# Kernel tuning notes

Measured on AMD Instinct MI355X. Metric: run time of the kernel, lower is better.

The kernel has to match this reference:

```python
import jax, jax.numpy as jnp
import numpy as np

INPUT_SIZE = 20
HIDDEN = 51
OUT = 1
B = 4096
T = 512


def _init_lstm_params(key, in_dim, hid_dim):
    # PyTorch LSTMCell init: U(-1/sqrt(hid), 1/sqrt(hid))
    k = 1.0 / np.sqrt(hid_dim)
    ks = jax.random.split(key, 4)
    W_ih = jax.random.uniform(ks[0], (4 * hid_dim, in_dim), minval=-k, maxval=k, dtype=jnp.float32)
    W_hh = jax.random.uniform(ks[1], (4 * hid_dim, hid_dim), minval=-k, maxval=k, dtype=jnp.float32)
    b_ih = jax.random.uniform(ks[2], (4 * hid_dim,), minval=-k, maxval=k, dtype=jnp.float32)
    b_hh = jax.random.uniform(ks[3], (4 * hid_dim,), minval=-k, maxval=k, dtype=jnp.float32)
    return W_ih, W_hh, b_ih, b_hh


def setup_inputs() -> dict:
    key = jax.random.key(0)
    k_x, k1, k2, k3, k4 = jax.random.split(key, 5)
    x = jax.random.normal(k_x, (B, T, INPUT_SIZE), dtype=jnp.float32)
    W_ih1, W_hh1, b_ih1, b_hh1 = _init_lstm_params(k1, INPUT_SIZE, HIDDEN)
    W_ih2, W_hh2, b_ih2, b_hh2 = _init_lstm_params(k2, HIDDEN, OUT)
    kl = 1.0 / np.sqrt(OUT)
    ka, kb, kc, kd = jax.random.split(k3, 4)
    W_mu = jax.random.uniform(ka, (OUT, OUT), minval=-kl, maxval=kl, dtype=jnp.float32)
    b_mu = jax.random.uniform(kb, (OUT,), minval=-kl, maxval=kl, dtype=jnp.float32)
    W_lv = jax.random.uniform(kc, (OUT, OUT), minval=-kl, maxval=kl, dtype=jnp.float32)
    b_lv = jax.random.uniform(kd, (OUT,), minval=-kl, maxval=kl, dtype=jnp.float32)
    return {
        "x": x,
        "W_ih1": W_ih1, "W_hh1": W_hh1, "b_ih1": b_ih1, "b_hh1": b_hh1,
        "W_ih2": W_ih2, "W_hh2": W_hh2, "b_ih2": b_ih2, "b_hh2": b_hh2,
        "W_mu": W_mu, "b_mu": b_mu, "W_lv": W_lv, "b_lv": b_lv,
    }


def _lstm_cell(x_t, h, c, W_ih, W_hh, b_ih, b_hh):
    # PyTorch LSTMCell: gate order i, f, g, o
    gates = x_t @ W_ih.T + b_ih + h @ W_hh.T + b_hh
    i, f, g, o = jnp.split(gates, 4, axis=-1)
    c_new = jax.nn.sigmoid(f) * c + jax.nn.sigmoid(i) * jnp.tanh(g)
    h_new = jax.nn.sigmoid(o) * jnp.tanh(c_new)
    return h_new, c_new


def reference(x, W_ih1, W_hh1, b_ih1, b_hh1, W_ih2, W_hh2, b_ih2, b_hh2, W_mu, b_mu, W_lv, b_lv):
    bsz = x.shape[0]
    h1 = jnp.zeros((bsz, HIDDEN), dtype=x.dtype)
    c1 = jnp.zeros((bsz, HIDDEN), dtype=x.dtype)
    h2 = jnp.zeros((bsz, OUT), dtype=x.dtype)
    c2 = jnp.zeros((bsz, OUT), dtype=x.dtype)

    def step(carry, x_t):
        h1, c1, h2, c2 = carry
        h1, c1 = _lstm_cell(x_t, h1, c1, W_ih1, W_hh1, b_ih1, b_hh1)
        h2, c2 = _lstm_cell(h1, h2, c2, W_ih2, W_hh2, b_ih2, b_hh2)
        return (h1, c1, h2, c2), h2

    xs = jnp.swapaxes(x, 0, 1)  # [T, B, input_size]
    _, h2_seq = jax.lax.scan(step, (h1, c1, h2, c2), xs)  # h2_seq: [T, B, 1]
    agg = jnp.mean(h2_seq, axis=0)  # [B, 1] mean over time
    mu = agg @ W_mu.T + b_mu
    log_var = agg @ W_lv.T + b_lv
    sigma = jnp.exp(0.5 * log_var)
    lower = mu - 1.96 * sigma
    upper = mu + 1.96 * sigma
    return (lower, mu, upper, log_var)
```

## Files before the change

### kernel.cpp

```cpp
#include <hip/hip_runtime.h>

#define B_TOT 4096
#define T_STEPS 512
#define IN 20
#define HID 51

typedef float f32x4 __attribute__((ext_vector_type(4)));
typedef short s16x8 __attribute__((ext_vector_type(8)));

__device__ __forceinline__ unsigned short f2bf(float f) {
    unsigned int u = __float_as_uint(f);
    unsigned int r = (u + 0x7fffu + ((u >> 16) & 1u)) >> 16;
    return (unsigned short)r;
}

__device__ __forceinline__ float fast_rcp(float x) { return __builtin_amdgcn_rcpf(x); }
__device__ __forceinline__ float sigf(float x) { return fast_rcp(1.0f + __expf(-x)); }
__device__ __forceinline__ float tanh_(float x) { return 1.0f - 2.0f * fast_rcp(1.0f + __expf(2.0f * x)); }


__global__ __launch_bounds__(512, 2)
void lstm_fused(const float* __restrict__ x,
                const float* __restrict__ Wih1, const float* __restrict__ Whh1,
                const float* __restrict__ bih1, const float* __restrict__ bhh1,
                const float* __restrict__ Wih2, const float* __restrict__ Whh2,
                const float* __restrict__ bih2, const float* __restrict__ bhh2,
                const float* __restrict__ Wmu,  const float* __restrict__ bmu,
                const float* __restrict__ Wlv,  const float* __restrict__ blv,
                float* __restrict__ out)
{
    __shared__ __align__(16) unsigned short vA[2][3][64][8];

    const int tid  = threadIdx.x;
    const int lane = tid & 63;
    const int w    = tid >> 6;
    const int bidx = blockIdx.x;

    const int ntile = (w < 6) ? 2 : 1;
    int tiles[2];
    tiles[0] = (w < 6) ? 2 * w : (w == 6 ? 12 : 13);
    tiles[1] = (w < 6) ? 2 * w + 1 : -1;
    const bool isL2 = (tiles[0] == 13);

    s16x8 wfrag[2][3];
    float bias[2][4];
    #pragma unroll
    for (int ti = 0; ti < 2; ++ti) {
        const int tau = tiles[ti];
        const int m = lane & 15;
        #pragma unroll
        for (int ks = 0; ks < 3; ++ks) {
            s16x8 f;
            #pragma unroll
            for (int j = 0; j < 8; ++j) {
                int k = ks * 32 + ((lane >> 4) << 3) + j;
                float v = 0.0f;
                if (tau >= 0) {
                    if (tau < 13) {
                        int g = m & 3, unit = tau * 4 + (m >> 2);
                        if (unit < HID) {
                            int row = g * HID + unit;
                            if (k < IN) v = Wih1[row * IN + k];
                            else if (k >= 32 && k < 32 + HID) v = Whh1[row * HID + (k - 32)];
                        }
                    } else {
                        if (m < 4 && k >= 32 && k < 32 + HID) v = Wih2[m * HID + (k - 32)];
                    }
                }
                f[j] = (short)f2bf(v);
            }
            wfrag[ti][ks] = f;
        }
        #pragma unroll
        for (int r = 0; r < 4; ++r) {
            float bv = 0.0f;
            if (tau >= 0 && tau < 13) {
                int unit = tau * 4 + (lane >> 4);
                if (unit < HID) bv = bih1[r * HID + unit] + bhh1[r * HID + unit];
            }
            bias[ti][r] = bv;
        }
    }

    float whh2g[4], b2g[4];
    #pragma unroll
    for (int r = 0; r < 4; ++r) { whh2g[r] = Whh2[r]; b2g[r] = bih2[r] + bhh2[r]; }

    const bool xs = (tid < 16 * IN);
    const int xb = tid / IN, xm = tid % IN;
    const float* xp = x + ((size_t)(bidx * 16 + xb) * T_STEPS) * IN + xm;
    const int xrow = ((xm >> 3) & 3) * 16 + xb;
    const int xj = xm & 7;

    {
        unsigned short* vz = &vA[0][0][0][0];
        for (int i = tid; i < 2 * 3 * 64 * 8; i += 512) vz[i] = 0;
    }
    __syncthreads();
    if (xs) vA[0][0][xrow][xj] = f2bf(xp[0]);
    __syncthreads();

    float c1[2] = {0.f, 0.f};
    float c2p = 0.f, h2p = 0.f, sum2 = 0.f;

    for (int t = 0; t < T_STEPS; ++t) {
        const int p  = t & 1;
        const int pn = p ^ 1;

        const int t1 = (t < T_STEPS - 1) ? t + 1 : t;
        float xr = 0.0f;
        if (xs) xr = xp[(size_t)t1 * IN];

        s16x8 bf0 = *(const s16x8*)&vA[p][0][lane][0];
        s16x8 bf1 = *(const s16x8*)&vA[p][1][lane][0];
        s16x8 bf2 = *(const s16x8*)&vA[p][2][lane][0];

        f32x4 acc[2];
        {
            f32x4 a = {0.f, 0.f, 0.f, 0.f};
            a = __builtin_amdgcn_mfma_f32_16x16x32_bf16(wfrag[0][0], bf0, a, 0, 0, 0);
            a = __builtin_amdgcn_mfma_f32_16x16x32_bf16(wfrag[0][1], bf1, a, 0, 0, 0);
            a = __builtin_amdgcn_mfma_f32_16x16x32_bf16(wfrag[0][2], bf2, a, 0, 0, 0);
            acc[0] = a;
        }
        if (ntile == 2) {
            f32x4 a = {0.f, 0.f, 0.f, 0.f};
            a = __builtin_amdgcn_mfma_f32_16x16x32_bf16(wfrag[1][0], bf0, a, 0, 0, 0);
            a = __builtin_amdgcn_mfma_f32_16x16x32_bf16(wfrag[1][1], bf1, a, 0, 0, 0);
            a = __builtin_amdgcn_mfma_f32_16x16x32_bf16(wfrag[1][2], bf2, a, 0, 0, 0);
            acc[1] = a;
        }

        #pragma unroll
        for (int ti = 0; ti < 2; ++ti) {
            if (ti < ntile && tiles[ti] < 13) {
                float gi = acc[ti][0] + bias[ti][0];
                float gf = acc[ti][1] + bias[ti][1];
                float gg = acc[ti][2] + bias[ti][2];
                float go = acc[ti][3] + bias[ti][3];
                float c  = sigf(gf) * c1[ti] + sigf(gi) * tanh_(gg);
                c1[ti]   = c;
                float h  = sigf(go) * tanh_(c);
                int unit = tiles[ti] * 4 + (lane >> 4);
                int k    = 32 + unit;
                int b    = lane & 15;
                vA[pn][k >> 5][(((k >> 3) & 3) << 4) + b][k & 7] = f2bf(h);
            }
        }

        if (isL2 && t > 0 && lane < 16) {
            float pi = acc[0][0] + b2g[0] + whh2g[0] * h2p;
            float pf = acc[0][1] + b2g[1] + whh2g[1] * h2p;
            float pg = acc[0][2] + b2g[2] + whh2g[2] * h2p;
            float po = acc[0][3] + b2g[3] + whh2g[3] * h2p;
            float c2 = sigf(pf) * c2p + sigf(pi) * tanh_(pg);
            c2p = c2;
            h2p = sigf(po) * tanh_(c2);
            sum2 += h2p;
        }

        if (xs) vA[pn][0][xrow][xj] = f2bf(xr);

        __syncthreads();
    }

    if (isL2) {
        s16x8 bf0 = *(const s16x8*)&vA[0][0][lane][0];
        s16x8 bf1 = *(const s16x8*)&vA[0][1][lane][0];
        s16x8 bf2 = *(const s16x8*)&vA[0][2][lane][0];
        f32x4 a = {0.f, 0.f, 0.f, 0.f};
        a = __builtin_amdgcn_mfma_f32_16x16x32_bf16(wfrag[0][0], bf0, a, 0, 0, 0);
        a = __builtin_amdgcn_mfma_f32_16x16x32_bf16(wfrag[0][1], bf1, a, 0, 0, 0);
        a = __builtin_amdgcn_mfma_f32_16x16x32_bf16(wfrag[0][2], bf2, a, 0, 0, 0);
        if (lane < 16) {
            float pi = a[0] + b2g[0] + whh2g[0] * h2p;
            float pf = a[1] + b2g[1] + whh2g[1] * h2p;
            float pg = a[2] + b2g[2] + whh2g[2] * h2p;
            float po = a[3] + b2g[3] + whh2g[3] * h2p;
            float c2 = sigf(pf) * c2p + sigf(pi) * tanh_(pg);
            h2p = sigf(po) * tanh_(c2);
            sum2 += h2p;

            float agg = sum2 * (1.0f / 512.0f);
            float mu  = Wmu[0] * agg + bmu[0];
            float lv  = Wlv[0] * agg + blv[0];
            float sg  = __expf(0.5f * lv);
            int bg = bidx * 16 + lane;
            out[bg]             = mu - 1.96f * sg;
            out[B_TOT + bg]     = mu;
            out[2 * B_TOT + bg] = mu + 1.96f * sg;
            out[3 * B_TOT + bg] = lv;
        }
    }
}

extern "C" void kernel_launch(void* const* d_in, const int* in_sizes, int n_in,
                              void* d_out, int out_size, void* d_ws, size_t ws_size,
                              hipStream_t stream) {
    const float* x    = (const float*)d_in[0];
    const float* Wih1 = (const float*)d_in[1];
    const float* Whh1 = (const float*)d_in[2];
    const float* bih1 = (const float*)d_in[3];
    const float* bhh1 = (const float*)d_in[4];
    const float* Wih2 = (const float*)d_in[5];
    const float* Whh2 = (const float*)d_in[6];
    const float* bih2 = (const float*)d_in[7];
    const float* bhh2 = (const float*)d_in[8];
    const float* Wmu  = (const float*)d_in[9];
    const float* bmu  = (const float*)d_in[10];
    const float* Wlv  = (const float*)d_in[11];
    const float* blv  = (const float*)d_in[12];
    float* out = (float*)d_out;

    lstm_fused<<<dim3(B_TOT / 16), dim3(512), 0, stream>>>(
        x, Wih1, Whh1, bih1, bhh1, Wih2, Whh2, bih2, bhh2, Wmu, bmu, Wlv, blv, out);
}
```

Measured before the change: 505.0 us.

## Use 1024-thread blocks with one gate tile per wave and dedicated x-loader waves

The block grows from 512 to 1024 threads. Each of 13 waves now owns a single layer-1 gate tile, one wave handles layer 2, and two extra waves stage x into LDS with a two-step-ahead prefetch. Bias is folded into the MFMA accumulator init, and layer 2 skips the zero-weight K-slice. The aim is to shorten the serial per-step critical path by removing the second tile per wave. In exchange occupancy drops to one block per launch-bounds setting, and the per-step barrier now spans 16 waves.

New measurement: 671.2 us. 32.9% more time.

```diff
diff --git a/kernel.cpp b/kernel.cpp
--- a/kernel.cpp
+++ b/kernel.cpp
@@ -19,7 +19,7 @@
 __device__ __forceinline__ float tanh_(float x) { return 1.0f - 2.0f * fast_rcp(1.0f + __expf(2.0f * x)); }
 
 
-__global__ __launch_bounds__(512, 2)
+__global__ __launch_bounds__(1024, 1)
 void lstm_fused(const float* __restrict__ x,
                 const float* __restrict__ Wih1, const float* __restrict__ Whh1,
                 const float* __restrict__ bih1, const float* __restrict__ bhh1,
@@ -36,147 +36,138 @@
     const int w    = tid >> 6;
     const int bidx = blockIdx.x;
 
-    const int ntile = (w < 6) ? 2 : 1;
-    int tiles[2];
-    tiles[0] = (w < 6) ? 2 * w : (w == 6 ? 12 : 13);
-    tiles[1] = (w < 6) ? 2 * w + 1 : -1;
-    const bool isL2 = (tiles[0] == 13);
-
-    s16x8 wfrag[2][3];
-    float bias[2][4];
+    const int tau = (w < 13) ? w : (w == 13 ? 13 : -1);
+    const bool isL1 = (tau >= 0 && tau < 13);
+    const bool isL2 = (tau == 13);
+
+    s16x8 wfrag[3];
     #pragma unroll
-    for (int ti = 0; ti < 2; ++ti) {
-        const int tau = tiles[ti];
+    for (int ks = 0; ks < 3; ++ks) {
+        s16x8 f;
         const int m = lane & 15;
         #pragma unroll
-        for (int ks = 0; ks < 3; ++ks) {
-            s16x8 f;
+        for (int j = 0; j < 8; ++j) {
+            int k = ks * 32 + ((lane >> 4) << 3) + j;
+            float v = 0.0f;
+            if (isL1) {
+                int g = m & 3, unit = tau * 4 + (m >> 2);
+                if (unit < HID) {
+                    int row = g * HID + unit;
+                    if (k < IN) v = Wih1[row * IN + k];
+                    else if (k >= 32 && k < 32 + HID) v = Whh1[row * HID + (k - 32)];
+                }
+            } else if (isL2) {
+                if (m < 4 && k >= 32 && k < 32 + HID) v = Wih2[m * HID + (k - 32)];
+            }
+            f[j] = (short)f2bf(v);
+        }
+        wfrag[ks] = f;
+    }
+
+    f32x4 binit = {0.f, 0.f, 0.f, 0.f};
+    if (isL1) {
+        int unit = tau * 4 + (lane >> 4);
+        if (unit < HID) {
             #pragma unroll
-            for (int j = 0; j < 8; ++j) {
-                int k = ks * 32 + ((lane >> 4) << 3) + j;
-                float v = 0.0f;
-                if (tau >= 0) {
-                    if (tau < 13) {
-                        int g = m & 3, unit = tau * 4 + (m >> 2);
-                        if (unit < HID) {
-                            int row = g * HID + unit;
-                            if (k < IN) v = Wih1[row * IN + k];
-                            else if (k >= 32 && k < 32 + HID) v = Whh1[row * HID + (k - 32)];
-                        }
-                    } else {
-                        if (m < 4 && k >= 32 && k < 32 + HID) v = Wih2[m * HID + (k - 32)];
-                    }
-                }
-                f[j] = (short)f2bf(v);
-            }
-            wfrag[ti][ks] = f;
-        }
+            for (int r = 0; r < 4; ++r) binit[r] = bih1[r * HID + unit] + bhh1[r * HID + unit];
+        }
+    }
+    float whh2g[4];
+    if (isL2) {
         #pragma unroll
-        for (int r = 0; r < 4; ++r) {
-            float bv = 0.0f;
-            if (tau >= 0 && tau < 13) {
-                int unit = tau * 4 + (lane >> 4);
-                if (unit < HID) bv = bih1[r * HID + unit] + bhh1[r * HID + unit];
-            }
-            bias[ti][r] = bv;
-        }
-    }
-
-    float whh2g[4], b2g[4];
+        for (int r = 0; r < 4; ++r) { whh2g[r] = Whh2[r]; binit[r] = bih2[r] + bhh2[r]; }
+    }
+
+    const int s = tid - 14 * 64;
+    const bool st = (s >= 0);
+    int  se[3];  bool sv[3];  const float* sp[3];  int srow[3], sj[3];
     #pragma unroll
-    for (int r = 0; r < 4; ++r) { whh2g[r] = Whh2[r]; b2g[r] = bih2[r] + bhh2[r]; }
-
-    const bool xs = (tid < 16 * IN);
-    const int xb = tid / IN, xm = tid % IN;
-    const float* xp = x + ((size_t)(bidx * 16 + xb) * T_STEPS) * IN + xm;
-    const int xrow = ((xm >> 3) & 3) * 16 + xb;
-    const int xj = xm & 7;
+    for (int i = 0; i < 3; ++i) {
+        se[i] = s + i * 128;
+        sv[i] = st && se[i] < 16 * IN;
+        if (sv[i]) {
+            int b = se[i] / IN, m = se[i] % IN;
+            sp[i]   = x + ((size_t)(bidx * 16 + b) * T_STEPS) * IN + m;
+            srow[i] = ((m >> 3) & 3) * 16 + b;
+            sj[i]   = m & 7;
+        } else { sp[i] = x; srow[i] = 0; sj[i] = 0; }
+    }
 
     {
         unsigned short* vz = &vA[0][0][0][0];
-        for (int i = tid; i < 2 * 3 * 64 * 8; i += 512) vz[i] = 0;
+        for (int i = tid; i < 2 * 3 * 64 * 8; i += 1024) vz[i] = 0;
     }
     __syncthreads();
-    if (xs) vA[0][0][xrow][xj] = f2bf(xp[0]);
+    float xr[3] = {0.f, 0.f, 0.f};
+    #pragma unroll
+    for (int i = 0; i < 3; ++i) if (sv[i]) {
+        vA[0][0][srow[i]][sj[i]] = f2bf(sp[i][0]);
+        xr[i] = sp[i][(T_STEPS > 1) ? IN : 0];
+    }
     __syncthreads();
 
-    float c1[2] = {0.f, 0.f};
+    float c1 = 0.f;
     float c2p = 0.f, h2p = 0.f, sum2 = 0.f;
 
     for (int t = 0; t < T_STEPS; ++t) {
         const int p  = t & 1;
         const int pn = p ^ 1;
 
-        const int t1 = (t < T_STEPS - 1) ? t + 1 : t;
-        float xr = 0.0f;
-        if (xs) xr = xp[(size_t)t1 * IN];
-
-        s16x8 bf0 = *(const s16x8*)&vA[p][0][lane][0];
-        s16x8 bf1 = *(const s16x8*)&vA[p][1][lane][0];
-        s16x8 bf2 = *(const s16x8*)&vA[p][2][lane][0];
-
-        f32x4 acc[2];
-        {
-            f32x4 a = {0.f, 0.f, 0.f, 0.f};
-            a = __builtin_amdgcn_mfma_f32_16x16x32_bf16(wfrag[0][0], bf0, a, 0, 0, 0);
-            a = __builtin_amdgcn_mfma_f32_16x16x32_bf16(wfrag[0][1], bf1, a, 0, 0, 0);
-            a = __builtin_amdgcn_mfma_f32_16x16x32_bf16(wfrag[0][2], bf2, a, 0, 0, 0);
-            acc[0] = a;
-        }
-        if (ntile == 2) {
-            f32x4 a = {0.f, 0.f, 0.f, 0.f};
-            a = __builtin_amdgcn_mfma_f32_16x16x32_bf16(wfrag[1][0], bf0, a, 0, 0, 0);
-            a = __builtin_amdgcn_mfma_f32_16x16x32_bf16(wfrag[1][1], bf1, a, 0, 0, 0);
-            a = __builtin_amdgcn_mfma_f32_16x16x32_bf16(wfrag[1][2], bf2, a, 0, 0, 0);
-            acc[1] = a;
-        }
-
-        #pragma unroll
-        for (int ti = 0; ti < 2; ++ti) {
-            if (ti < ntile && tiles[ti] < 13) {
-                float gi = acc[ti][0] + bias[ti][0];
-                float gf = acc[ti][1] + bias[ti][1];
-                float gg = acc[ti][2] + bias[ti][2];
-                float go = acc[ti][3] + bias[ti][3];
-                float c  = sigf(gf) * c1[ti] + sigf(gi) * tanh_(gg);
-                c1[ti]   = c;
-                float h  = sigf(go) * tanh_(c);
-                int unit = tiles[ti] * 4 + (lane >> 4);
-                int k    = 32 + unit;
-                int b    = lane & 15;
-                vA[pn][k >> 5][(((k >> 3) & 3) << 4) + b][k & 7] = f2bf(h);
+        if (isL1) {
+            s16x8 bf0 = *(const s16x8*)&vA[p][0][lane][0];
+            s16x8 bf1 = *(const s16x8*)&vA[p][1][lane][0];
+            s16x8 bf2 = *(const s16x8*)&vA[p][2][lane][0];
+            f32x4 a = binit;
+            a = __builtin_amdgcn_mfma_f32_16x16x32_bf16(wfrag[0], bf0, a, 0, 0, 0);
+            a = __builtin_amdgcn_mfma_f32_16x16x32_bf16(wfrag[1], bf1, a, 0, 0, 0);
+            a = __builtin_amdgcn_mfma_f32_16x16x32_bf16(wfrag[2], bf2, a, 0, 0, 0);
+
+            float c  = sigf(a[1]) * c1 + sigf(a[0]) * tanh_(a[2]);
+            c1 = c;
+            float h  = sigf(a[3]) * tanh_(c);
+            int unit = tau * 4 + (lane >> 4);
+            int k    = 32 + unit;
+            int b    = lane & 15;
+            vA[pn][k >> 5][(((k >> 3) & 3) << 4) + b][k & 7] = f2bf(h);
+        } else if (isL2) {
+            s16x8 bf1 = *(const s16x8*)&vA[p][1][lane][0];
+            s16x8 bf2 = *(const s16x8*)&vA[p][2][lane][0];
+            f32x4 a = binit;
+            a = __builtin_amdgcn_mfma_f32_16x16x32_bf16(wfrag[1], bf1, a, 0, 0, 0);
+            a = __builtin_amdgcn_mfma_f32_16x16x32_bf16(wfrag[2], bf2, a, 0, 0, 0);
+            if (t > 0 && lane < 16) {
+                float pi = a[0] + whh2g[0] * h2p;
+                float pf = a[1] + whh2g[1] * h2p;
+                float pg = a[2] + whh2g[2] * h2p;
+                float po = a[3] + whh2g[3] * h2p;
+                float c2 = sigf(pf) * c2p + sigf(pi) * tanh_(pg);
+                c2p = c2;
+                h2p = sigf(po) * tanh_(c2);
+                sum2 += h2p;
             }
-        }
-
-        if (isL2 && t > 0 && lane < 16) {
-            float pi = acc[0][0] + b2g[0] + whh2g[0] * h2p;
-            float pf = acc[0][1] + b2g[1] + whh2g[1] * h2p;
-            float pg = acc[0][2] + b2g[2] + whh2g[2] * h2p;
-            float po = acc[0][3] + b2g[3] + whh2g[3] * h2p;
-            float c2 = sigf(pf) * c2p + sigf(pi) * tanh_(pg);
-            c2p = c2;
-            h2p = sigf(po) * tanh_(c2);
-            sum2 += h2p;
-        }
-
-        if (xs) vA[pn][0][xrow][xj] = f2bf(xr);
+        } else {
+            const int t2 = (t < T_STEPS - 2) ? t + 2 : T_STEPS - 1;
+            #pragma unroll
+            for (int i = 0; i < 3; ++i) if (sv[i]) {
+                vA[pn][0][srow[i]][sj[i]] = f2bf(xr[i]);
+                xr[i] = sp[i][(size_t)t2 * IN];
+            }
+        }
 
         __syncthreads();
     }
 
     if (isL2) {
-        s16x8 bf0 = *(const s16x8*)&vA[0][0][lane][0];
         s16x8 bf1 = *(const s16x8*)&vA[0][1][lane][0];
         s16x8 bf2 = *(const s16x8*)&vA[0][2][lane][0];
-        f32x4 a = {0.f, 0.f, 0.f, 0.f};
-        a = __builtin_amdgcn_mfma_f32_16x16x32_bf16(wfrag[0][0], bf0, a, 0, 0, 0);
-        a = __builtin_amdgcn_mfma_f32_16x16x32_bf16(wfrag[0][1], bf1, a, 0, 0, 0);
-        a = __builtin_amdgcn_mfma_f32_16x16x32_bf16(wfrag[0][2], bf2, a, 0, 0, 0);
+        f32x4 a = binit;
+        a = __builtin_amdgcn_mfma_f32_16x16x32_bf16(wfrag[1], bf1, a, 0, 0, 0);
+        a = __builtin_amdgcn_mfma_f32_16x16x32_bf16(wfrag[2], bf2, a, 0, 0, 0);
         if (lane < 16) {
-            float pi = a[0] + b2g[0] + whh2g[0] * h2p;
-            float pf = a[1] + b2g[1] + whh2g[1] * h2p;
-            float pg = a[2] + b2g[2] + whh2g[2] * h2p;
-            float po = a[3] + b2g[3] + whh2g[3] * h2p;
+            float pi = a[0] + whh2g[0] * h2p;
+            float pf = a[1] + whh2g[1] * h2p;
+            float pg = a[2] + whh2g[2] * h2p;
+            float po = a[3] + whh2g[3] * h2p;
             float c2 = sigf(pf) * c2p + sigf(pi) * tanh_(pg);
             h2p = sigf(po) * tanh_(c2);
             sum2 += h2p;
@@ -212,6 +203,6 @@
     const float* blv  = (const float*)d_in[12];
     float* out = (float*)d_out;
 
-    lstm_fused<<<dim3(B_TOT / 16), dim3(512), 0, stream>>>(
+    lstm_fused<<<dim3(B_TOT / 16), dim3(1024), 0, stream>>>(
         x, Wih1, Whh1, bih1, bhh1, Wih2, Whh2, bih2, bhh2, Wmu, bmu, Wlv, blv, out);
 }
```
